# Performance work log

Measured on AMD Instinct MI355X. Metric: run time of the kernel, lower is better.

The kernel has to match this reference:

```python
import jax, jax.numpy as jnp
import numpy as np

N = 50000
E = 800000
D_IN = 128
D_OUT = 128
LN_EPS = 1e-5
DROP_P = 0.1


def setup_inputs() -> dict:
    key = jax.random.key(0)
    ks = jax.random.split(key, 8)
    x = jax.random.normal(ks[0], (N, D_IN), dtype=jnp.float32)
    edge_index = jax.random.randint(ks[1], (2, E), 0, N, dtype=jnp.int64)
    # dropout mask: binary keep-mask scaled by 1/(1-p), as torch dropout produces
    u = jax.random.uniform(ks[2], (N, D_IN), dtype=jnp.float32)
    dropout_mask = (u > DROP_P).astype(jnp.float32) / (1.0 - DROP_P)
    # LayerNorm affine params
    gamma = jnp.ones((D_IN,), dtype=jnp.float32)
    beta = jnp.zeros((D_IN,), dtype=jnp.float32)
    # SAGEConv linears: lin_l (aggregated neighbors, with bias), lin_r (root, no bias)
    s = 1.0 / np.sqrt(D_IN)
    w_l = jax.random.uniform(ks[3], (D_OUT, D_IN), minval=-s, maxval=s, dtype=jnp.float32)
    b_l = jax.random.uniform(ks[4], (D_OUT,), minval=-s, maxval=s, dtype=jnp.float32)
    w_r = jax.random.uniform(ks[5], (D_OUT, D_IN), minval=-s, maxval=s, dtype=jnp.float32)
    return {"x": x, "edge_index": edge_index, "dropout_mask": dropout_mask,
            "gamma": gamma, "beta": beta, "w_l": w_l, "b_l": b_l, "w_r": w_r}


def reference(x, edge_index, dropout_mask, gamma, beta, w_l, b_l, w_r):
    # LayerNorm + ReLU + dropout mask
    mu = jnp.mean(x, axis=-1, keepdims=True)
    var = jnp.mean(jnp.square(x - mu), axis=-1, keepdims=True)
    h = (x - mu) * jax.lax.rsqrt(var + LN_EPS) * gamma + beta
    h = jax.nn.relu(h) * dropout_mask  # [N, D_IN]
    # SAGEConv: mean-aggregate source features into target nodes
    src = edge_index[0]
    dst = edge_index[1]
    msg = h[src]  # [E, D_IN] gathered messages
    agg = jax.ops.segment_sum(msg, dst, num_segments=N)  # [N, D_IN]
    deg = jax.ops.segment_sum(jnp.ones((E,), dtype=h.dtype), dst, num_segments=N)
    agg = agg / jnp.maximum(deg, 1.0)[:, None]
    # out = lin_l(agg) + lin_r(h)
    out = agg @ w_l.T + b_l + h @ w_r.T  # [N, D_OUT]
    return out
```

## Files before the change

### kernel.cpp

```cpp
#include <hip/hip_runtime.h>
#include <hip/hip_bf16.h>

#define N_NODES 50000
#define N_EDGES 800000
#define D 128
#define NB_SCAN ((N_NODES + 255) / 256)

__device__ __forceinline__ unsigned int bf16u(float f) {
  __hip_bfloat16 b = __float2bfloat16(f);
  return (unsigned int)*reinterpret_cast<unsigned short*>(&b);
}

__global__ __launch_bounds__(256) void ln_kernel(
    const float* __restrict__ x, const float* __restrict__ mask,
    const float* __restrict__ gamma, const float* __restrict__ beta,
    float* __restrict__ h) {
  const int l = threadIdx.x & 63;
  const int n = blockIdx.x * 4 + (threadIdx.x >> 6);
  const float2 xv = ((const float2*)x)[(size_t)n * 64 + l];
  float s = xv.x + xv.y;
  float q = xv.x * xv.x + xv.y * xv.y;
#pragma unroll
  for (int m = 1; m < 64; m <<= 1) {
    s += __shfl_xor(s, m);
    q += __shfl_xor(q, m);
  }
  const float mean = s * (1.0f / 128.0f);
  const float var = q * (1.0f / 128.0f) - mean * mean;
  const float rs = rsqrtf(var + 1e-5f);
  const float2 gv = ((const float2*)gamma)[l];
  const float2 bv = ((const float2*)beta)[l];
  const float2 mv = ((const float2*)mask)[(size_t)n * 64 + l];
  float2 hv;
  hv.x = fmaxf((xv.x - mean) * rs * gv.x + bv.x, 0.0f) * mv.x;
  hv.y = fmaxf((xv.y - mean) * rs * gv.y + bv.y, 0.0f) * mv.y;
  ((float2*)h)[(size_t)n * 64 + l] = hv;
}

__global__ __launch_bounds__(256) void wt_kernel(
    const float* __restrict__ w_l, const float* __restrict__ w_r,
    float* __restrict__ wt) {
  const int i = blockIdx.x * 256 + threadIdx.x;
  const int k = i >> 8;
  const int d = i & 255;
  wt[i] = (d < D) ? w_l[d * D + k] : w_r[(d - D) * D + k];
}

__global__ __launch_bounds__(256) void gemm_kernel(
    const float* __restrict__ h, const float* __restrict__ wt,
    const float* __restrict__ b_l, unsigned int* __restrict__ gb,
    float* __restrict__ r) {
  __shared__ __align__(16) float As[32][32];
  __shared__ __align__(16) float Ws[32 * 256];
  const int t = threadIdx.x;
  const int tx = t & 31;
  const int ty = t >> 5;
  const int nb = blockIdx.x * 32;
  float acc[4][8];
#pragma unroll
  for (int i = 0; i < 4; ++i)
#pragma unroll
    for (int j = 0; j < 8; ++j) acc[i][j] = 0.0f;

  for (int c = 0; c < 4; ++c) {
    const int k0 = c * 32;
    {
      const int node = t >> 3;
      const int kk = (t & 7) * 4;
      int n = nb + node;
      if (n >= N_NODES) n = N_NODES - 1;
      const float4 v = *(const float4*)(h + (size_t)n * D + k0 + kk);
      As[kk + 0][node] = v.x;
      As[kk + 1][node] = v.y;
      As[kk + 2][node] = v.z;
      As[kk + 3][node] = v.w;
    }
    {
      const float4* src = (const float4*)(wt + (size_t)k0 * 256);
      float4* dstp = (float4*)(&Ws[0]);
#pragma unroll
      for (int i = 0; i < 8; ++i) dstp[t + 256 * i] = src[t + 256 * i];
    }
    __syncthreads();
#pragma unroll
    for (int kk = 0; kk < 32; ++kk) {
      const float4 a = *(const float4*)(&As[kk][ty * 4]);
      const float4 w0 = *(const float4*)(&Ws[kk * 256 + tx * 4]);
      const float4 w1 = *(const float4*)(&Ws[kk * 256 + 128 + tx * 4]);
      const float av[4] = {a.x, a.y, a.z, a.w};
#pragma unroll
      for (int i = 0; i < 4; ++i) {
        acc[i][0] += av[i] * w0.x;
        acc[i][1] += av[i] * w0.y;
        acc[i][2] += av[i] * w0.z;
        acc[i][3] += av[i] * w0.w;
        acc[i][4] += av[i] * w1.x;
        acc[i][5] += av[i] * w1.y;
        acc[i][6] += av[i] * w1.z;
        acc[i][7] += av[i] * w1.w;
      }
    }
    __syncthreads();
  }
  const float4 bv = ((const float4*)b_l)[tx];
#pragma unroll
  for (int i = 0; i < 4; ++i) {
    const int n = nb + ty * 4 + i;
    if (n < N_NODES) {
      uint2 gp;
      gp.x = (bf16u(acc[i][1]) << 16) | bf16u(acc[i][0]);
      gp.y = (bf16u(acc[i][3]) << 16) | bf16u(acc[i][2]);
      ((uint2*)gb)[(size_t)n * 32 + tx] = gp;
      float4 rv;
      rv.x = acc[i][4] + bv.x; rv.y = acc[i][5] + bv.y;
      rv.z = acc[i][6] + bv.z; rv.w = acc[i][7] + bv.w;
      *(float4*)(r + (size_t)n * D + tx * 4) = rv;
    }
  }
}

__global__ __launch_bounds__(256) void hist_kernel(const int* __restrict__ ei,
                                                   int* __restrict__ deg,
                                                   int* __restrict__ rank) {
  const int e = blockIdx.x * 256 + threadIdx.x;
  if (e < N_EDGES) rank[e] = atomicAdd(&deg[ei[N_EDGES + e]], 1);
}

__global__ __launch_bounds__(256) void scan1_kernel(
    const int* __restrict__ deg, int* __restrict__ offsets,
    int* __restrict__ partial) {
  __shared__ int sm[256];
  const int t = threadIdx.x;
  const int i = blockIdx.x * 256 + t;
  const int v = (i < N_NODES) ? deg[i] : 0;
  sm[t] = v;
  __syncthreads();
#pragma unroll
  for (int ofs = 1; ofs < 256; ofs <<= 1) {
    int x = sm[t];
    if (t >= ofs) x += sm[t - ofs];
    __syncthreads();
    sm[t] = x;
    __syncthreads();
  }
  if (i < N_NODES) offsets[i] = sm[t] - v;
  if (t == 255) partial[blockIdx.x] = sm[255];
}

__global__ __launch_bounds__(256) void scan2_kernel(int* __restrict__ partial) {
  __shared__ int sm[256];
  const int t = threadIdx.x;
  const int v = (t < NB_SCAN) ? partial[t] : 0;
  sm[t] = v;
  __syncthreads();
#pragma unroll
  for (int ofs = 1; ofs < 256; ofs <<= 1) {
    int x = sm[t];
    if (t >= ofs) x += sm[t - ofs];
    __syncthreads();
    sm[t] = x;
    __syncthreads();
  }
  if (t < NB_SCAN) partial[t] = sm[t] - v;
}

__global__ __launch_bounds__(256) void scan3_kernel(
    int* __restrict__ offsets, const int* __restrict__ partial) {
  const int i = blockIdx.x * 256 + threadIdx.x;
  if (i < N_NODES) offsets[i] += partial[blockIdx.x];
  if (i == 0) offsets[N_NODES] = N_EDGES;
}

__global__ __launch_bounds__(256) void scatter_kernel(
    const int* __restrict__ ei, const int* __restrict__ offsets,
    const int* __restrict__ rank, int* __restrict__ csr) {
  const int e = blockIdx.x * 256 + threadIdx.x;
  if (e < N_EDGES) {
    const int dst = ei[N_EDGES + e];
    csr[offsets[dst] + rank[e]] = ei[e];
  }
}

#define ACC8(v)                                  \
  do {                                           \
    acc[0] += __uint_as_float((v).x << 16);      \
    acc[1] += __uint_as_float((v).x & 0xffff0000u); \
    acc[2] += __uint_as_float((v).y << 16);      \
    acc[3] += __uint_as_float((v).y & 0xffff0000u); \
    acc[4] += __uint_as_float((v).z << 16);      \
    acc[5] += __uint_as_float((v).z & 0xffff0000u); \
    acc[6] += __uint_as_float((v).w << 16);      \
    acc[7] += __uint_as_float((v).w & 0xffff0000u); \
  } while (0)

__global__ __launch_bounds__(256) void agg_kernel(
    const int* __restrict__ offsets, const int* __restrict__ csr,
    const unsigned int* __restrict__ gb, const float* __restrict__ r,
    float* __restrict__ out) {
  const int l = threadIdx.x & 63;
  const int q = l >> 4;
  const int c = l & 15;
  const int n = blockIdx.x * 4 + (threadIdx.x >> 6);
  const int s = offsets[n];
  const int e = offsets[n + 1];
  const uint4* g4 = (const uint4*)gb;
  float acc[8];
#pragma unroll
  for (int k = 0; k < 8; ++k) acc[k] = 0.0f;
  for (int base = s; base < e; base += 64) {
    const int cnt = min(e - base, 64);
    int idx = (l < cnt) ? csr[base + l] : 0;
    int j = 0;
    for (; j + 16 <= cnt; j += 16) {
      const int i0 = __shfl(idx, j + 0 + q);
      const int i1 = __shfl(idx, j + 4 + q);
      const int i2 = __shfl(idx, j + 8 + q);
      const int i3 = __shfl(idx, j + 12 + q);
      const uint4 v0 = g4[(size_t)i0 * 16 + c];
      const uint4 v1 = g4[(size_t)i1 * 16 + c];
      const uint4 v2 = g4[(size_t)i2 * 16 + c];
      const uint4 v3 = g4[(size_t)i3 * 16 + c];
      ACC8(v0);
      ACC8(v1);
      ACC8(v2);
      ACC8(v3);
    }
    for (; j + 4 <= cnt; j += 4) {
      const int i0 = __shfl(idx, j + q);
      const uint4 v0 = g4[(size_t)i0 * 16 + c];
      ACC8(v0);
    }
    if (j < cnt) {
      const int rem = cnt - j;
      const int i0 = __shfl(idx, j + min(q, rem - 1));
      if (q < rem) {
        const uint4 v0 = g4[(size_t)i0 * 16 + c];
        ACC8(v0);
      }
    }
  }
#pragma unroll
  for (int k = 0; k < 8; ++k) {
    acc[k] += __shfl_xor(acc[k], 16);
    acc[k] += __shfl_xor(acc[k], 32);
  }
  if (l < 16) {
    const float inv = 1.0f / fmaxf((float)(e - s), 1.0f);
    const float4 r0 = ((const float4*)r)[(size_t)n * 32 + c * 2 + 0];
    const float4 r1 = ((const float4*)r)[(size_t)n * 32 + c * 2 + 1];
    float4 o0, o1;
    o0.x = fmaf(acc[0], inv, r0.x);
    o0.y = fmaf(acc[1], inv, r0.y);
    o0.z = fmaf(acc[2], inv, r0.z);
    o0.w = fmaf(acc[3], inv, r0.w);
    o1.x = fmaf(acc[4], inv, r1.x);
    o1.y = fmaf(acc[5], inv, r1.y);
    o1.z = fmaf(acc[6], inv, r1.z);
    o1.w = fmaf(acc[7], inv, r1.w);
    ((float4*)out)[(size_t)n * 32 + c * 2 + 0] = o0;
    ((float4*)out)[(size_t)n * 32 + c * 2 + 1] = o1;
  }
}

extern "C" void kernel_launch(void* const* d_in, const int* in_sizes, int n_in,
                              void* d_out, int out_size, void* d_ws,
                              size_t ws_size, hipStream_t stream) {
  const float* x = (const float*)d_in[0];
  const int* ei = (const int*)d_in[1];
  const float* mask = (const float*)d_in[2];
  const float* gamma = (const float*)d_in[3];
  const float* beta = (const float*)d_in[4];
  const float* w_l = (const float*)d_in[5];
  const float* b_l = (const float*)d_in[6];
  const float* w_r = (const float*)d_in[7];
  float* out = (float*)d_out;

  char* ws = (char*)d_ws;
  size_t off = 0;
  auto alloc = [&](size_t bytes) {
    char* p = ws + off;
    off += (bytes + 255) & ~(size_t)255;
    return p;
  };
  float* h = (float*)alloc((size_t)N_NODES * D * sizeof(float));
  unsigned int* gb =
      (unsigned int*)alloc((size_t)N_NODES * D * sizeof(unsigned short));
  float* r = (float*)alloc((size_t)N_NODES * D * sizeof(float));
  float* wt = (float*)alloc((size_t)2 * D * D * sizeof(float));
  int* deg = (int*)alloc((size_t)N_NODES * sizeof(int));
  int* offsets = (int*)alloc((size_t)(N_NODES + 1) * sizeof(int));
  int* partial = (int*)alloc((size_t)NB_SCAN * sizeof(int));
  int* rank = (int*)alloc((size_t)N_EDGES * sizeof(int));
  int* csr = (int*)alloc((size_t)N_EDGES * sizeof(int));

  hipMemsetAsync(deg, 0, (size_t)N_NODES * sizeof(int), stream);
  wt_kernel<<<(2 * D * D) / 256, 256, 0, stream>>>(w_l, w_r, wt);
  ln_kernel<<<N_NODES / 4, 256, 0, stream>>>(x, mask, gamma, beta, h);
  gemm_kernel<<<(N_NODES + 31) / 32, 256, 0, stream>>>(h, wt, b_l, gb, r);
  hist_kernel<<<N_EDGES / 256, 256, 0, stream>>>(ei, deg, rank);
  scan1_kernel<<<NB_SCAN, 256, 0, stream>>>(deg, offsets, partial);
  scan2_kernel<<<1, 256, 0, stream>>>(partial);
  scan3_kernel<<<NB_SCAN, 256, 0, stream>>>(offsets, partial);
  scatter_kernel<<<N_EDGES / 256, 256, 0, stream>>>(ei, offsets, rank, csr);
  agg_kernel<<<N_NODES / 4, 256, 0, stream>>>(offsets, csr, gb, r, out);
}
```

Measured before the change: 255.3 us.

## Use bf16 MFMA for node linear transforms with bf16 activations and weights

Rewrites the dense projection so it runs on 16x16x32 bf16 MFMA instructions instead of fp32 FMA loops. LayerNorm output and the weights are stored as bf16, which halves the memory traffic for h. The grid is split over 4 column tiles of 64 and results are staged through LDS before coalesced stores. This lowers the precision of the root term and of the aggregated projections, and each column block reloads the A tile.

```diff
diff --git a/kernel.cpp b/kernel.cpp
--- a/kernel.cpp
+++ b/kernel.cpp
@@ -6,6 +6,9 @@
 #define D 128
 #define NB_SCAN ((N_NODES + 255) / 256)
 
+typedef short bf16x8 __attribute__((ext_vector_type(8)));
+typedef float f32x4 __attribute__((ext_vector_type(4)));
+
 __device__ __forceinline__ unsigned int bf16u(float f) {
   __hip_bfloat16 b = __float2bfloat16(f);
   return (unsigned int)*reinterpret_cast<unsigned short*>(&b);
@@ -14,7 +17,7 @@
 __global__ __launch_bounds__(256) void ln_kernel(
     const float* __restrict__ x, const float* __restrict__ mask,
     const float* __restrict__ gamma, const float* __restrict__ beta,
-    float* __restrict__ h) {
+    unsigned int* __restrict__ hb) {
   const int l = threadIdx.x & 63;
   const int n = blockIdx.x * 4 + (threadIdx.x >> 6);
   const float2 xv = ((const float2*)x)[(size_t)n * 64 + l];
@@ -31,90 +34,99 @@
   const float2 gv = ((const float2*)gamma)[l];
   const float2 bv = ((const float2*)beta)[l];
   const float2 mv = ((const float2*)mask)[(size_t)n * 64 + l];
-  float2 hv;
-  hv.x = fmaxf((xv.x - mean) * rs * gv.x + bv.x, 0.0f) * mv.x;
-  hv.y = fmaxf((xv.y - mean) * rs * gv.y + bv.y, 0.0f) * mv.y;
-  ((float2*)h)[(size_t)n * 64 + l] = hv;
+  const float h0 = fmaxf((xv.x - mean) * rs * gv.x + bv.x, 0.0f) * mv.x;
+  const float h1 = fmaxf((xv.y - mean) * rs * gv.y + bv.y, 0.0f) * mv.y;
+  hb[(size_t)n * 64 + l] = (bf16u(h1) << 16) | bf16u(h0);
 }
 
 __global__ __launch_bounds__(256) void wt_kernel(
     const float* __restrict__ w_l, const float* __restrict__ w_r,
-    float* __restrict__ wt) {
+    unsigned int* __restrict__ wtb) {
   const int i = blockIdx.x * 256 + threadIdx.x;
-  const int k = i >> 8;
-  const int d = i & 255;
-  wt[i] = (d < D) ? w_l[d * D + k] : w_r[(d - D) * D + k];
+  const float* src = (i < 8192) ? w_l : w_r;
+  const int j = (i < 8192) ? 2 * i : 2 * (i - 8192);
+  wtb[i] = (bf16u(src[j + 1]) << 16) | bf16u(src[j]);
 }
 
 __global__ __launch_bounds__(256) void gemm_kernel(
-    const float* __restrict__ h, const float* __restrict__ wt,
+    const unsigned short* __restrict__ hb, const unsigned short* __restrict__ wtb,
     const float* __restrict__ b_l, unsigned int* __restrict__ gb,
     float* __restrict__ r) {
-  __shared__ __align__(16) float As[32][32];
-  __shared__ __align__(16) float Ws[32 * 256];
+  __shared__ float lds[64][65];
   const int t = threadIdx.x;
-  const int tx = t & 31;
-  const int ty = t >> 5;
-  const int nb = blockIdx.x * 32;
-  float acc[4][8];
-#pragma unroll
-  for (int i = 0; i < 4; ++i)
-#pragma unroll
-    for (int j = 0; j < 8; ++j) acc[i][j] = 0.0f;
-
-  for (int c = 0; c < 4; ++c) {
-    const int k0 = c * 32;
-    {
-      const int node = t >> 3;
-      const int kk = (t & 7) * 4;
-      int n = nb + node;
-      if (n >= N_NODES) n = N_NODES - 1;
-      const float4 v = *(const float4*)(h + (size_t)n * D + k0 + kk);
-      As[kk + 0][node] = v.x;
-      As[kk + 1][node] = v.y;
-      As[kk + 2][node] = v.z;
-      As[kk + 3][node] = v.w;
-    }
-    {
-      const float4* src = (const float4*)(wt + (size_t)k0 * 256);
-      float4* dstp = (float4*)(&Ws[0]);
-#pragma unroll
-      for (int i = 0; i < 8; ++i) dstp[t + 256 * i] = src[t + 256 * i];
-    }
-    __syncthreads();
-#pragma unroll
-    for (int kk = 0; kk < 32; ++kk) {
-      const float4 a = *(const float4*)(&As[kk][ty * 4]);
-      const float4 w0 = *(const float4*)(&Ws[kk * 256 + tx * 4]);
-      const float4 w1 = *(const float4*)(&Ws[kk * 256 + 128 + tx * 4]);
-      const float av[4] = {a.x, a.y, a.z, a.w};
-#pragma unroll
-      for (int i = 0; i < 4; ++i) {
-        acc[i][0] += av[i] * w0.x;
-        acc[i][1] += av[i] * w0.y;
-        acc[i][2] += av[i] * w0.z;
-        acc[i][3] += av[i] * w0.w;
-        acc[i][4] += av[i] * w1.x;
-        acc[i][5] += av[i] * w1.y;
-        acc[i][6] += av[i] * w1.z;
-        acc[i][7] += av[i] * w1.w;
+  const int w = t >> 6;
+  const int l = t & 63;
+  const int lm = l & 15;
+  const int quad = l >> 4;
+  const int nb = blockIdx.x * 64;
+  const int by = blockIdx.y;
+
+  int anode = nb + w * 16 + lm;
+  if (anode >= N_NODES) anode = N_NODES - 1;
+  const unsigned short* arow = hb + (size_t)anode * D + quad * 8;
+  bf16x8 af[4];
+#pragma unroll
+  for (int ch = 0; ch < 4; ++ch)
+    af[ch] = *(const bf16x8*)(arow + ch * 32);
+
+  const unsigned short* brow = wtb + (size_t)(by * 64 + lm) * D + quad * 8;
+  bf16x8 bf[4][4];
+#pragma unroll
+  for (int sub = 0; sub < 4; ++sub)
+#pragma unroll
+    for (int ch = 0; ch < 4; ++ch)
+      bf[sub][ch] = *(const bf16x8*)(brow + sub * 16 * D + ch * 32);
+
+  f32x4 acc[4];
+#pragma unroll
+  for (int sub = 0; sub < 4; ++sub) acc[sub] = (f32x4){0.f, 0.f, 0.f, 0.f};
+#pragma unroll
+  for (int ch = 0; ch < 4; ++ch)
+#pragma unroll
+    for (int sub = 0; sub < 4; ++sub)
+      acc[sub] = __builtin_amdgcn_mfma_f32_16x16x32_bf16(af[ch], bf[sub][ch],
+                                                         acc[sub], 0, 0, 0);
+
+#pragma unroll
+  for (int sub = 0; sub < 4; ++sub)
+#pragma unroll
+    for (int reg = 0; reg < 4; ++reg)
+      lds[w * 16 + quad * 4 + reg][sub * 16 + lm] = acc[sub][reg];
+  __syncthreads();
+
+  if (by < 2) {
+#pragma unroll
+    for (int i = 0; i < 2; ++i) {
+      const int row = (t >> 3) + i * 32;
+      const int grp = t & 7;
+      const int node = nb + row;
+      if (node < N_NODES) {
+        const float* lr = &lds[row][grp * 8];
+        uint4 p;
+        p.x = (bf16u(lr[1]) << 16) | bf16u(lr[0]);
+        p.y = (bf16u(lr[3]) << 16) | bf16u(lr[2]);
+        p.z = (bf16u(lr[5]) << 16) | bf16u(lr[4]);
+        p.w = (bf16u(lr[7]) << 16) | bf16u(lr[6]);
+        ((uint4*)gb)[(size_t)node * 16 + by * 8 + grp] = p;
       }
     }
-    __syncthreads();
-  }
-  const float4 bv = ((const float4*)b_l)[tx];
-#pragma unroll
-  for (int i = 0; i < 4; ++i) {
-    const int n = nb + ty * 4 + i;
-    if (n < N_NODES) {
-      uint2 gp;
-      gp.x = (bf16u(acc[i][1]) << 16) | bf16u(acc[i][0]);
-      gp.y = (bf16u(acc[i][3]) << 16) | bf16u(acc[i][2]);
-      ((uint2*)gb)[(size_t)n * 32 + tx] = gp;
-      float4 rv;
-      rv.x = acc[i][4] + bv.x; rv.y = acc[i][5] + bv.y;
-      rv.z = acc[i][6] + bv.z; rv.w = acc[i][7] + bv.w;
-      *(float4*)(r + (size_t)n * D + tx * 4) = rv;
+  } else {
+    const int row = t >> 2;
+    const int grp = t & 3;
+    const int node = nb + row;
+    const int col0 = (by - 2) * 64 + grp * 16;
+    if (node < N_NODES) {
+#pragma unroll
+      for (int qd = 0; qd < 4; ++qd) {
+        const float4 bv = *(const float4*)(b_l + col0 + qd * 4);
+        const float* lr = &lds[row][grp * 16 + qd * 4];
+        float4 o;
+        o.x = lr[0] + bv.x;
+        o.y = lr[1] + bv.y;
+        o.z = lr[2] + bv.z;
+        o.w = lr[3] + bv.w;
+        *(float4*)(r + (size_t)node * D + col0 + qd * 4) = o;
+      }
     }
   }
 }
@@ -181,15 +193,15 @@
   }
 }
 
-#define ACC8(v)                                  \
-  do {                                           \
-    acc[0] += __uint_as_float((v).x << 16);      \
+#define ACC8(v)                                     \
+  do {                                              \
+    acc[0] += __uint_as_float((v).x << 16);         \
     acc[1] += __uint_as_float((v).x & 0xffff0000u); \
-    acc[2] += __uint_as_float((v).y << 16);      \
+    acc[2] += __uint_as_float((v).y << 16);         \
     acc[3] += __uint_as_float((v).y & 0xffff0000u); \
-    acc[4] += __uint_as_float((v).z << 16);      \
+    acc[4] += __uint_as_float((v).z << 16);         \
     acc[5] += __uint_as_float((v).z & 0xffff0000u); \
-    acc[6] += __uint_as_float((v).w << 16);      \
+    acc[6] += __uint_as_float((v).w << 16);         \
     acc[7] += __uint_as_float((v).w & 0xffff0000u); \
   } while (0)
 
@@ -282,11 +294,13 @@
     off += (bytes + 255) & ~(size_t)255;
     return p;
   };
-  float* h = (float*)alloc((size_t)N_NODES * D * sizeof(float));
+  unsigned int* hb =
+      (unsigned int*)alloc((size_t)N_NODES * D * sizeof(unsigned short));
   unsigned int* gb =
       (unsigned int*)alloc((size_t)N_NODES * D * sizeof(unsigned short));
   float* r = (float*)alloc((size_t)N_NODES * D * sizeof(float));
-  float* wt = (float*)alloc((size_t)2 * D * D * sizeof(float));
+  unsigned int* wtb =
+      (unsigned int*)alloc((size_t)2 * D * D * sizeof(unsigned short));
   int* deg = (int*)alloc((size_t)N_NODES * sizeof(int));
   int* offsets = (int*)alloc((size_t)(N_NODES + 1) * sizeof(int));
   int* partial = (int*)alloc((size_t)NB_SCAN * sizeof(int));
@@ -294,9 +308,10 @@
   int* csr = (int*)alloc((size_t)N_EDGES * sizeof(int));
 
   hipMemsetAsync(deg, 0, (size_t)N_NODES * sizeof(int), stream);
-  wt_kernel<<<(2 * D * D) / 256, 256, 0, stream>>>(w_l, w_r, wt);
-  ln_kernel<<<N_NODES / 4, 256, 0, stream>>>(x, mask, gamma, beta, h);
-  gemm_kernel<<<(N_NODES + 31) / 32, 256, 0, stream>>>(h, wt, b_l, gb, r);
+  wt_kernel<<<64, 256, 0, stream>>>(w_l, w_r, wtb);
+  ln_kernel<<<N_NODES / 4, 256, 0, stream>>>(x, mask, gamma, beta, hb);
+  gemm_kernel<<<dim3((N_NODES + 63) / 64, 4), 256, 0, stream>>>(
+      (const unsigned short*)hb, (const unsigned short*)wtb, b_l, gb, r);
   hist_kernel<<<N_EDGES / 256, 256, 0, stream>>>(ei, deg, rank);
   scan1_kernel<<<NB_SCAN, 256, 0, stream>>>(deg, offsets, partial);
   scan2_kernel<<<1, 256, 0, stream>>>(partial);
```

New measurement: 240.3 us. 5.9% less time.
